# Kernel tuning notes

Hardware: AMD Instinct MI355X
Metric: run time of the kernel (lower is better)

The kernel has to match this reference:

```python
import jax, jax.numpy as jnp
import numpy as np

DT = 0.1
K = 262144


def _skew(v):
    # v: [k,3] -> [k,3,3]
    x, y, z = v[..., 0], v[..., 1], v[..., 2]
    O = jnp.zeros_like(x)
    return jnp.stack([
        jnp.stack([O, -z, y], -1),
        jnp.stack([z, O, -x], -1),
        jnp.stack([-y, x, O], -1)], -2)


def _se3_exp(t):
    # t: [k,6] twist = [rho(linear), phi(angular)] -> (R [k,3,3], p [k,3])
    rho, phi = t[:, :3], t[:, 3:]
    th2 = jnp.sum(phi * phi, -1)
    small = th2 < 1e-8
    th2s = jnp.where(small, 1.0, th2)        # safe denominator
    th = jnp.sqrt(th2s)
    A = jnp.where(small, 1.0 - th2 / 6.0, jnp.sin(th) / th)
    B = jnp.where(small, 0.5 - th2 / 24.0, (1.0 - jnp.cos(th)) / th2s)
    C = jnp.where(small, 1.0 / 6.0 - th2 / 120.0, (th - jnp.sin(th)) / (th2s * th))
    S = _skew(phi)
    S2 = S @ S
    I = jnp.eye(3, dtype=t.dtype)
    R = I + A[:, None, None] * S + B[:, None, None] * S2
    V = I + B[:, None, None] * S + C[:, None, None] * S2
    p = jnp.einsum('kij,kj->ki', V, rho)
    return R, p


def _adjoint(R, p):
    # SE3 adjoint for twist order [linear, angular]: [[R, [p]x R],[0, R]]
    top = jnp.concatenate([R, _skew(p) @ R], -1)
    bot = jnp.concatenate([jnp.zeros_like(R), R], -1)
    return jnp.concatenate([top, bot], -2)  # [k,6,6]


def setup_inputs() -> dict:
    key = jax.random.key(0)
    ks = jax.random.split(key, 8)
    s = jax.random.normal(ks[0], (K, 1, 18), dtype=jnp.float32) * 0.1
    # state layout: [pos(3), rot(9), twist(6)]; rotation must be a valid R (identity, as in fake_state)
    s = s.at[:, :, 3:12].set(jnp.eye(3, dtype=jnp.float32).reshape(9))
    a = jax.random.normal(ks[1], (K, 1, 6), dtype=jnp.float32) * 0.1
    h0 = jnp.zeros((1, K, 12), dtype=jnp.float32)
    W_ih = jax.random.normal(ks[2], (12, 21), dtype=jnp.float32) / np.sqrt(21)
    W_hh = jax.random.normal(ks[3], (12, 12), dtype=jnp.float32) / np.sqrt(12)
    W1 = jax.random.normal(ks[4], (128, 12), dtype=jnp.float32) / np.sqrt(12)
    W2 = jax.random.normal(ks[5], (128, 128), dtype=jnp.float32) / np.sqrt(128)
    W3 = jax.random.normal(ks[6], (6, 128), dtype=jnp.float32) / np.sqrt(128)
    return {"s": s, "a": a, "h0": h0, "W_ih": W_ih, "W_hh": W_hh, "W1": W1, "W2": W2, "W3": W3}


def reference(s, a, h0, W_ih, W_hh, W1, W2, W3):
    k = s.shape[0]
    # RNN input: pose-rot+vel (cols 3:) concat action -> [k, 21] (tau=1)
    x = jnp.concatenate([s[:, :, 3:], a], -1)[:, 0]
    h1 = jnp.tanh(x @ W_ih.T + h0[0] @ W_hh.T)          # [k,12] single RNN step, no bias
    hN = h1[None]                                        # [1,k,12]
    lrelu = lambda z: jnp.where(z >= 0, z, 0.1 * z)
    dv = lrelu(lrelu(h1 @ W1.T) @ W2.T) @ W3.T           # [k,6]
    v = s[:, -1, -6:]                                    # body twist
    p = s[:, -1, :3]
    R = s[:, -1, 3:12].reshape(k, 3, 3)
    # SE3 integration: M_next = M_current @ Exp(v*dt)
    Re, pe = _se3_exp(v * DT)
    R_next = R @ Re
    p_next = jnp.einsum('kij,kj->ki', R, pe) + p
    # M_next^-1
    Rinv = jnp.swapaxes(R_next, -1, -2)
    pinv = -jnp.einsum('kij,kj->ki', Rinv, p_next)
    # velocity update through adjoints
    vI = jnp.einsum('kij,kj->ki', _adjoint(R, p), v)
    v_next = jnp.einsum('kij,kj->ki', _adjoint(Rinv, pinv), vI + dv)
    s_next = jnp.concatenate([p_next, R_next.reshape(k, 9), v_next], -1)[:, None, :]
    return s_next, hN, dv
```

## Files before the change

### kernel.cpp

```cpp
#include <hip/hip_runtime.h>
#include <math.h>

typedef __attribute__((ext_vector_type(8))) short short8;
typedef __attribute__((ext_vector_type(4))) float f32x4;

#define DT_STEP 0.1f

static __device__ __forceinline__ unsigned bf16rne(float f) {
    unsigned u = __builtin_bit_cast(unsigned, f);
    return (u + 0x7fffu + ((u >> 16) & 1u)) >> 16;
}
static __device__ __forceinline__ unsigned bf16pk2(float lo, float hi) {
    unsigned r;
    asm("v_cvt_pk_bf16_f32 %0, %1, %2" : "=v"(r) : "v"(lo), "v"(hi));
    return r;
}
static __device__ __forceinline__ float tanh_fast(float v) {
    float e = __expf(2.0f * v);
    return 1.0f - 2.0f / (e + 1.0f);
}

static __device__ __forceinline__ uint4 tr_read8(unsigned a) {
    uint2 lo, hi;
    asm volatile("ds_read_b64_tr_b16 %0, %2 offset:0\n\t"
                 "ds_read_b64_tr_b16 %1, %2 offset:128"
                 : "=&v"(lo), "=&v"(hi) : "v"(a));
    return make_uint4(lo.x, lo.y, hi.x, hi.y);
}

static __device__ __forceinline__ void mm3(const float* A, const float* B, float* C) {
#pragma unroll
    for (int i = 0; i < 3; ++i)
#pragma unroll
        for (int j = 0; j < 3; ++j)
            C[i * 3 + j] = A[i * 3 + 0] * B[0 * 3 + j] + A[i * 3 + 1] * B[1 * 3 + j] + A[i * 3 + 2] * B[2 * 3 + j];
}
static __device__ __forceinline__ void mv3(const float* A, const float* x, float* y) {
#pragma unroll
    for (int i = 0; i < 3; ++i) y[i] = A[i * 3 + 0] * x[0] + A[i * 3 + 1] * x[1] + A[i * 3 + 2] * x[2];
}
static __device__ __forceinline__ void mtv3(const float* A, const float* x, float* y) {
#pragma unroll
    for (int i = 0; i < 3; ++i) y[i] = A[0 * 3 + i] * x[0] + A[1 * 3 + i] * x[1] + A[2 * 3 + i] * x[2];
}
static __device__ __forceinline__ void cross3(const float* p, const float* u, float* y) {
    y[0] = p[1] * u[2] - p[2] * u[1];
    y[1] = p[2] * u[0] - p[0] * u[2];
    y[2] = p[0] * u[1] - p[1] * u[0];
}

__global__ __launch_bounds__(256)
void weights_prep(const float* __restrict__ W1, const float* __restrict__ W2,
                  const float* __restrict__ W3, unsigned short* __restrict__ ws) {
    int i = blockIdx.x * 256 + threadIdx.x;
    if (i < 4096) {
        int n = i >> 5, k = i & 31;
        ws[i] = (k < 12) ? (unsigned short)bf16rne(W1[n * 12 + k]) : (unsigned short)0;
    } else if (i < 20480) {
        ws[i] = (unsigned short)bf16rne(W2[i - 4096]);
    } else if (i < 22528) {
        int j = i - 20480;
        int jj = j & 7;
        int l = (j >> 3) & 15;
        int kl = j >> 7;
        int k = kl * 8 + jj;
        ws[i] = (l < 6) ? (unsigned short)bf16rne(W3[l * 128 + k]) : (unsigned short)0;
    }
}

__global__ __launch_bounds__(64, 3)
void auv_mfma7_kernel(const float* __restrict__ s, const float* __restrict__ a,
                      const float* __restrict__ h0, const float* __restrict__ W_ih,
                      const float* __restrict__ W_hh, const unsigned short* __restrict__ Wbf,
                      float* __restrict__ out, int K)
{
    __shared__ __align__(16) char lds[16384];
    const int lane = threadIdx.x & 63;
    const int l15  = lane & 15;
    const int lg   = lane >> 4;

    char* l12 = &lds[0];
    char* h1t = &lds[0];
    char* dvt = &lds[0];

    const unsigned trb   = (unsigned)(lg * 256 + l15 * 8);
    const unsigned stoff = ((l15 >> 2) << 7) + ((l15 & 3) << 5) + (lg << 3);

    const unsigned short* W1A = Wbf;
    const unsigned short* W2B = Wbf + 4096;
    const unsigned short* W3B = Wbf + 20480;

    const int e_raw = blockIdx.x * 64 + lane;
    const int e  = e_raw < K ? e_raw : K - 1;
    const bool live = e_raw < K;

    const float* srow = s  + (size_t)e * 18;
    const float* arow = a  + (size_t)e * 6;
    const float* hrow = h0 + (size_t)e * 12;

    float xv[21];
#pragma unroll
    for (int i = 0; i < 15; ++i) xv[i] = srow[3 + i];
#pragma unroll
    for (int i = 0; i < 6; ++i)  xv[15 + i] = arow[i];
    float h0v[12];
#pragma unroll
    for (int i = 0; i < 12; ++i) h0v[i] = hrow[i];

    float h1v[12];
#pragma unroll
    for (int j = 0; j < 12; ++j) {
        float acc = 0.f;
        const float* wih = W_ih + j * 21;
#pragma unroll
        for (int i = 0; i < 21; ++i) acc = fmaf(wih[i], xv[i], acc);
        const float* whh = W_hh + j * 12;
#pragma unroll
        for (int i = 0; i < 12; ++i) acc = fmaf(whh[i], h0v[i], acc);
        h1v[j] = tanh_fast(acc);
    }

    if (live) {
        float4* h4 = (float4*)(out + (size_t)K * 18 + (size_t)e * 12);
        h4[0] = make_float4(h1v[0], h1v[1], h1v[2], h1v[3]);
        h4[1] = make_float4(h1v[4], h1v[5], h1v[6], h1v[7]);
        h4[2] = make_float4(h1v[8], h1v[9], h1v[10], h1v[11]);
    }

    short8 bfr[4];
#pragma unroll
    for (int kt = 0; kt < 4; ++kt)
        bfr[kt] = __builtin_bit_cast(short8,
            *(const uint4*)(W2B + (l15 * 128 + kt * 32 + lg * 8)));

    {
        unsigned p0 = bf16pk2(h1v[0], h1v[1]);
        unsigned p1 = bf16pk2(h1v[2], h1v[3]);
        unsigned p2 = bf16pk2(h1v[4], h1v[5]);
        unsigned p3 = bf16pk2(h1v[6], h1v[7]);
        unsigned p4 = bf16pk2(h1v[8], h1v[9]);
        unsigned p5 = bf16pk2(h1v[10], h1v[11]);
        int rq = (lane & 1) << 4;
        *(uint4*)(h1t + lane * 32 + (0 ^ rq))  = make_uint4(p0, p1, p2, p3);
        *(uint4*)(h1t + lane * 32 + (16 ^ rq)) = make_uint4(p4, p5, 0u, 0u);
    }
    asm volatile("s_waitcnt lgkmcnt(0)" ::: "memory");
    __builtin_amdgcn_sched_barrier(0);

    const short8 zfrag = {0, 0, 0, 0, 0, 0, 0, 0};

    short8 af1[4];
#pragma unroll
    for (int rt = 0; rt < 4; ++rt) {
        af1[rt] = zfrag;
        if (lg < 2) {
            int row = rt * 16 + l15;
            af1[rt] = __builtin_bit_cast(short8,
                *(const uint4*)(h1t + row * 32 + ((lg * 16) ^ ((row & 1) << 4))));
        }
    }
    asm volatile("s_waitcnt lgkmcnt(0)" ::: "memory");
    __builtin_amdgcn_sched_barrier(0);

#pragma unroll 1
    for (int nt = 0; nt < 8; ++nt) {
        short8 b1 = __builtin_bit_cast(short8,
            *(const uint4*)(W1A + ((nt * 16 + l15) * 32 + lg * 8)));
#pragma unroll
        for (int rt = 0; rt < 4; ++rt) {
            f32x4 z = {0.f, 0.f, 0.f, 0.f};
            f32x4 c1 = __builtin_amdgcn_mfma_f32_16x16x32_bf16(af1[rt], b1, z, 0, 0, 0);
            float v0 = fmaxf(c1[0], 0.1f * c1[0]);
            float v1 = fmaxf(c1[1], 0.1f * c1[1]);
            float v2 = fmaxf(c1[2], 0.1f * c1[2]);
            float v3 = fmaxf(c1[3], 0.1f * c1[3]);
            *(uint2*)(l12 + rt * 4096 + nt * 512 + stoff) =
                make_uint2(bf16pk2(v0, v1), bf16pk2(v2, v3));
        }
    }
    asm volatile("s_waitcnt lgkmcnt(0)" ::: "memory");
    __builtin_amdgcn_sched_barrier(0);

    short8 af2[4][4];
#pragma unroll
    for (int rt = 0; rt < 4; ++rt)
#pragma unroll
        for (int kt = 0; kt < 4; ++kt)
            af2[rt][kt] = __builtin_bit_cast(short8, tr_read8(trb + rt * 4096 + kt * 1024));
    asm volatile("s_waitcnt lgkmcnt(0)" ::: "memory");
    __builtin_amdgcn_sched_barrier(0);

#pragma unroll 1
    for (int nt = 0; nt < 8; ++nt) {
        short8 bnext[4];
        if (nt < 7) {
#pragma unroll
            for (int kt = 0; kt < 4; ++kt)
                bnext[kt] = __builtin_bit_cast(short8,
                    *(const uint4*)(W2B + (((nt + 1) * 16 + l15) * 128 + kt * 32 + lg * 8)));
        }
#pragma unroll
        for (int rt = 0; rt < 4; ++rt) {
            f32x4 c2 = {0.f, 0.f, 0.f, 0.f};
#pragma unroll
            for (int kt = 0; kt < 4; ++kt)
                c2 = __builtin_amdgcn_mfma_f32_16x16x32_bf16(af2[rt][kt], bfr[kt], c2, 0, 0, 0);
            float v0 = fmaxf(c2[0], 0.1f * c2[0]);
            float v1 = fmaxf(c2[1], 0.1f * c2[1]);
            float v2 = fmaxf(c2[2], 0.1f * c2[2]);
            float v3 = fmaxf(c2[3], 0.1f * c2[3]);
            *(uint2*)(l12 + rt * 4096 + nt * 512 + stoff) =
                make_uint2(bf16pk2(v0, v1), bf16pk2(v2, v3));
        }
#pragma unroll
        for (int kt = 0; kt < 4; ++kt) bfr[kt] = bnext[kt];
    }
    asm volatile("s_waitcnt lgkmcnt(0)" ::: "memory");
    __builtin_amdgcn_sched_barrier(0);

    short8 af3[4][4];
#pragma unroll
    for (int rt = 0; rt < 4; ++rt)
#pragma unroll
        for (int kt = 0; kt < 4; ++kt)
            af3[rt][kt] = __builtin_bit_cast(short8, tr_read8(trb + rt * 4096 + kt * 1024));

    short8 b3f[4];
#pragma unroll
    for (int kt = 0; kt < 4; ++kt)
        b3f[kt] = __builtin_bit_cast(short8,
            *(const uint4*)(W3B + (((kt * 4 + lg) * 16 + l15) * 8)));

    float sv[18];
#pragma unroll
    for (int i = 0; i < 18; ++i) sv[i] = srow[i];
    const float* v = &sv[12];
    const float* p = &sv[0];
    const float* R = &sv[3];

    float Rn[9], pn[3], pinv[3], Rvl[3], Rva[3], px[3];
    {
        float rho[3] = {v[0] * DT_STEP, v[1] * DT_STEP, v[2] * DT_STEP};
        float phi[3] = {v[3] * DT_STEP, v[4] * DT_STEP, v[5] * DT_STEP};
        float th2 = phi[0] * phi[0] + phi[1] * phi[1] + phi[2] * phi[2];

        float A, B, C;
        if (th2 < 1e-8f) {
            A = 1.0f - th2 * (1.0f / 6.0f);
            B = 0.5f - th2 * (1.0f / 24.0f);
            C = (1.0f / 6.0f) - th2 * (1.0f / 120.0f);
        } else {
            float th = sqrtf(th2);
            float sn = sinf(th), cs = cosf(th);
            A = sn / th;
            B = (1.0f - cs) / th2;
            C = (th - sn) / (th2 * th);
        }

        float S[9] = {0.f, -phi[2], phi[1], phi[2], 0.f, -phi[0], -phi[1], phi[0], 0.f};
        float S2[9];
        mm3(S, S, S2);

        float Re[9], V[9];
#pragma unroll
        for (int i = 0; i < 9; ++i) {
            float I = (i == 0 || i == 4 || i == 8) ? 1.0f : 0.0f;
            Re[i] = I + A * S[i] + B * S2[i];
            V[i]  = I + B * S[i] + C * S2[i];
        }

        float pe[3];
        mv3(V, rho, pe);
        mm3(R, Re, Rn);
        mv3(R, pe, pn);
        pn[0] += p[0]; pn[1] += p[1]; pn[2] += p[2];

        mtv3(Rn, pn, pinv);
        pinv[0] = -pinv[0]; pinv[1] = -pinv[1]; pinv[2] = -pinv[2];

        mv3(R, &v[0], Rvl);
        mv3(R, &v[3], Rva);
        cross3(p, Rva, px);
    }

    asm volatile("s_waitcnt lgkmcnt(0)" ::: "memory");
    __builtin_amdgcn_sched_barrier(0);

    f32x4 c3[4];
#pragma unroll
    for (int rt = 0; rt < 4; ++rt) c3[rt] = (f32x4){0.f, 0.f, 0.f, 0.f};
#pragma unroll
    for (int kt = 0; kt < 4; ++kt) {
#pragma unroll
        for (int rt = 0; rt < 4; ++rt)
            c3[rt] = __builtin_amdgcn_mfma_f32_16x16x32_bf16(af3[rt][kt], b3f[kt], c3[rt], 0, 0, 0);
    }

    float dvv[6];
    if (l15 < 6) {
#pragma unroll
        for (int rt = 0; rt < 4; ++rt)
#pragma unroll
            for (int r = 0; r < 4; ++r) {
                int row = rt * 16 + lg * 4 + r;
                *(float*)(dvt + row * 32 + l15 * 4) = c3[rt][r];
            }
    }
    asm volatile("s_waitcnt lgkmcnt(0)" ::: "memory");
    __builtin_amdgcn_sched_barrier(0);
    {
        const float* dr = (const float*)(dvt + lane * 32);
        dvv[0] = dr[0]; dvv[1] = dr[1]; dvv[2] = dr[2];
        dvv[3] = dr[3]; dvv[4] = dr[4]; dvv[5] = dr[5];
    }

    float u6[6];
    u6[0] = Rvl[0] + px[0] + dvv[0];
    u6[1] = Rvl[1] + px[1] + dvv[1];
    u6[2] = Rvl[2] + px[2] + dvv[2];
    u6[3] = Rva[0] + dvv[3];
    u6[4] = Rva[1] + dvv[4];
    u6[5] = Rva[2] + dvv[5];

    float Rul[3], Rua[3];
    mtv3(Rn, &u6[0], Rul);
    mtv3(Rn, &u6[3], Rua);
    float pxu[3];
    cross3(pinv, Rua, pxu);
    float vn[6];
    vn[0] = Rul[0] + pxu[0];
    vn[1] = Rul[1] + pxu[1];
    vn[2] = Rul[2] + pxu[2];
    vn[3] = Rua[0];
    vn[4] = Rua[1];
    vn[5] = Rua[2];

    if (live) {
        float* s_next = out + (size_t)e * 18;
        s_next[0] = pn[0]; s_next[1] = pn[1]; s_next[2] = pn[2];
#pragma unroll
        for (int i = 0; i < 9; ++i) s_next[3 + i] = Rn[i];
#pragma unroll
        for (int i = 0; i < 6; ++i) s_next[12 + i] = vn[i];

        float* dvo = out + (size_t)K * 30 + (size_t)e * 6;
#pragma unroll
        for (int r = 0; r < 6; ++r) dvo[r] = dvv[r];
    }
}

extern "C" void kernel_launch(void* const* d_in, const int* in_sizes, int n_in,
                              void* d_out, int out_size, void* d_ws, size_t ws_size,
                              hipStream_t stream) {
    const float* s    = (const float*)d_in[0];
    const float* a    = (const float*)d_in[1];
    const float* h0   = (const float*)d_in[2];
    const float* W_ih = (const float*)d_in[3];
    const float* W_hh = (const float*)d_in[4];
    const float* W1   = (const float*)d_in[5];
    const float* W2   = (const float*)d_in[6];
    const float* W3   = (const float*)d_in[7];

    int K = in_sizes[0] / 18;
    unsigned short* ws = (unsigned short*)d_ws;

    weights_prep<<<(22528 + 255) / 256, 256, 0, stream>>>(W1, W2, W3, ws);

    int grid = (K + 63) / 64;
    auv_mfma7_kernel<<<grid, 64, 0, stream>>>(s, a, h0, W_ih, W_hh, ws,
                                              (float*)d_out, K);
}
```

Baseline: 53.20 us.

## Stage per-row inputs through LDS with coalesced float4 loads and reuse state registers

```diff
diff --git a/kernel.cpp b/kernel.cpp
--- a/kernel.cpp
+++ b/kernel.cpp
@@ -69,7 +69,7 @@
 }
 
 __global__ __launch_bounds__(64, 3)
-void auv_mfma7_kernel(const float* __restrict__ s, const float* __restrict__ a,
+void auv_mfma9_kernel(const float* __restrict__ s, const float* __restrict__ a,
                       const float* __restrict__ h0, const float* __restrict__ W_ih,
                       const float* __restrict__ W_hh, const unsigned short* __restrict__ Wbf,
                       float* __restrict__ out, int K)
@@ -80,7 +80,7 @@
     const int lg   = lane >> 4;
 
     char* l12 = &lds[0];
-    char* h1t = &lds[0];
+    char* h1t = &lds[9216];
     char* dvt = &lds[0];
 
     const unsigned trb   = (unsigned)(lg * 256 + l15 * 8);
@@ -90,22 +90,52 @@
     const unsigned short* W2B = Wbf + 4096;
     const unsigned short* W3B = Wbf + 20480;
 
-    const int e_raw = blockIdx.x * 64 + lane;
+    const int e0    = blockIdx.x * 64;
+    const int e_raw = e0 + lane;
     const int e  = e_raw < K ? e_raw : K - 1;
     const bool live = e_raw < K;
-
-    const float* srow = s  + (size_t)e * 18;
-    const float* arow = a  + (size_t)e * 6;
-    const float* hrow = h0 + (size_t)e * 12;
-
-    float xv[21];
-#pragma unroll
-    for (int i = 0; i < 15; ++i) xv[i] = srow[3 + i];
-#pragma unroll
-    for (int i = 0; i < 6; ++i)  xv[15 + i] = arow[i];
-    float h0v[12];
-#pragma unroll
-    for (int i = 0; i < 12; ++i) h0v[i] = hrow[i];
+    const bool full = (e0 + 64 <= K);
+
+    float xv[21], h0v[12], pv3[3];
+    if (full) {
+        const float4* sg = (const float4*)(s + (size_t)e0 * 18);
+        float4* st = (float4*)(lds + 0);
+#pragma unroll
+        for (int i = 0; i < 4; ++i) st[i * 64 + lane] = sg[i * 64 + lane];
+        if (lane < 32) st[256 + lane] = sg[256 + lane];
+        const float4* ag = (const float4*)(a + (size_t)e0 * 6);
+        float4* at = (float4*)(lds + 4608);
+        at[lane] = ag[lane];
+        if (lane < 32) at[64 + lane] = ag[64 + lane];
+        const float4* hg = (const float4*)(h0 + (size_t)e0 * 12);
+        float4* ht = (float4*)(lds + 6144);
+#pragma unroll
+        for (int i = 0; i < 3; ++i) ht[i * 64 + lane] = hg[i * 64 + lane];
+        asm volatile("s_waitcnt vmcnt(0) lgkmcnt(0)" ::: "memory");
+        __builtin_amdgcn_sched_barrier(0);
+
+        const float* sst = (const float*)(lds) + lane * 18;
+        pv3[0] = sst[0]; pv3[1] = sst[1]; pv3[2] = sst[2];
+#pragma unroll
+        for (int i = 0; i < 15; ++i) xv[i] = sst[3 + i];
+        const float* ast = (const float*)(lds + 4608) + lane * 6;
+#pragma unroll
+        for (int i = 0; i < 6; ++i) xv[15 + i] = ast[i];
+        const float* hst = (const float*)(lds + 6144) + lane * 12;
+#pragma unroll
+        for (int i = 0; i < 12; ++i) h0v[i] = hst[i];
+    } else {
+        const float* srow = s  + (size_t)e * 18;
+        const float* arow = a  + (size_t)e * 6;
+        const float* hrow = h0 + (size_t)e * 12;
+        pv3[0] = srow[0]; pv3[1] = srow[1]; pv3[2] = srow[2];
+#pragma unroll
+        for (int i = 0; i < 15; ++i) xv[i] = srow[3 + i];
+#pragma unroll
+        for (int i = 0; i < 6; ++i)  xv[15 + i] = arow[i];
+#pragma unroll
+        for (int i = 0; i < 12; ++i) h0v[i] = hrow[i];
+    }
 
     float h1v[12];
 #pragma unroll
@@ -190,6 +220,12 @@
     asm volatile("s_waitcnt lgkmcnt(0)" ::: "memory");
     __builtin_amdgcn_sched_barrier(0);
 
+    short8 b3f[4];
+#pragma unroll
+    for (int kt = 0; kt < 4; ++kt)
+        b3f[kt] = __builtin_bit_cast(short8,
+            *(const uint4*)(W3B + (((kt * 4 + lg) * 16 + l15) * 8)));
+
 #pragma unroll 1
     for (int nt = 0; nt < 8; ++nt) {
         short8 bnext[4];
@@ -225,18 +261,9 @@
         for (int kt = 0; kt < 4; ++kt)
             af3[rt][kt] = __builtin_bit_cast(short8, tr_read8(trb + rt * 4096 + kt * 1024));
 
-    short8 b3f[4];
-#pragma unroll
-    for (int kt = 0; kt < 4; ++kt)
-        b3f[kt] = __builtin_bit_cast(short8,
-            *(const uint4*)(W3B + (((kt * 4 + lg) * 16 + l15) * 8)));
-
-    float sv[18];
-#pragma unroll
-    for (int i = 0; i < 18; ++i) sv[i] = srow[i];
-    const float* v = &sv[12];
-    const float* p = &sv[0];
-    const float* R = &sv[3];
+    const float* v = &xv[9];
+    const float* p = pv3;
+    const float* R = &xv[0];
 
     float Rn[9], pn[3], pinv[3], Rvl[3], Rva[3], px[3];
     {
@@ -367,6 +394,6 @@
     weights_prep<<<(22528 + 255) / 256, 256, 0, stream>>>(W1, W2, W3, ws);
 
     int grid = (K + 63) / 64;
-    auv_mfma7_kernel<<<grid, 64, 0, stream>>>(s, a, h0, W_ih, W_hh, ws,
+    auv_mfma9_kernel<<<grid, 64, 0, stream>>>(s, a, h0, W_ih, W_hh, ws,
                                               (float*)d_out, K);
 }
```

Measured after the change: 55.61 us. 1.05x slower.
